# Performance work log

Measured on AMD Instinct MI355X. Metric: run time of the kernel, lower is better.

The kernel has to match this reference:

```python
import jax, jax.numpy as jnp
import numpy as np

B, N, D, KD = 8, 2048, 64, 64

def setup_inputs() -> dict:
    key = jax.random.key(0)
    ks = jax.random.split(key, 7)
    s = 1.0 / np.sqrt(D)
    return {
        "x":  jax.random.normal(ks[0], (B, N, D), dtype=jnp.float32),
        "Wq": jax.random.normal(ks[1], (D, KD), dtype=jnp.float32) * s,
        "bq": jnp.zeros((KD,), jnp.float32),
        "Wk": jax.random.normal(ks[2], (D, KD), dtype=jnp.float32) * s,
        "bk": jnp.zeros((KD,), jnp.float32),
        "Wv": jax.random.normal(ks[3], (D, KD), dtype=jnp.float32) * s,
        "bv": jnp.zeros((KD,), jnp.float32),
    }

def reference(x, Wq, bq, Wk, bk, Wv, bv):
    # Q,K,V: [B,N,KD]
    Q = x @ Wq + bq
    K = x @ Wk + bk
    V = x @ Wv + bv
    # scores: [B,N,N] (note: original applies NO 1/sqrt(d) scaling)
    scores = jnp.einsum('bij,bkj->bik', Q, K)
    probs = jax.nn.softmax(scores, axis=-1)
    # mean-threshold sparsification: keep entries above the row mean
    mask = (probs > jnp.mean(probs, axis=-1, keepdims=True)).astype(probs.dtype)
    sparse = probs * mask
    out = jnp.einsum('bij,bjk->bik', sparse, V)  # [B,N,KD]
    return out
```

## Files before the change

kernel.cpp:

```cpp
#include <hip/hip_runtime.h>

#define NB 8
#define NS 2048
#define ND 64
#define LOG2E 1.44269504f
#define QSC 256.0f
#define IQS (1.0f / 256.0f)

#define KST 80
#define VST 136
#define KTILE (128 * KST)
#define VTILE (64 * VST)

typedef _Float16 half8 __attribute__((ext_vector_type(8)));
typedef _Float16 half4 __attribute__((ext_vector_type(4)));
typedef __attribute__((ext_vector_type(4))) float floatx4;

__device__ __forceinline__ half8 cvt8(const float* p) {
    float4 a = *(const float4*)p;
    float4 b = *(const float4*)(p + 4);
    half8 h = {(_Float16)a.x, (_Float16)a.y, (_Float16)a.z, (_Float16)a.w,
               (_Float16)b.x, (_Float16)b.y, (_Float16)b.z, (_Float16)b.w};
    return h;
}

__global__ __launch_bounds__(256) void wprep(
    const float* __restrict__ Wq, const float* __restrict__ Wk,
    const float* __restrict__ Wv, _Float16* __restrict__ Wt)
{
    const int m = blockIdx.x;
    const float* W = (m == 0) ? Wq : (m == 1) ? Wk : Wv;
    for (int i = threadIdx.x; i < 64 * 64; i += 256) {
        const int c = i >> 6, d = i & 63;
        Wt[((size_t)m * 64 + c) * 64 + d] = (_Float16)W[d * 64 + c];
    }
}

__global__ __launch_bounds__(256) void qkv_proj(
    const float* __restrict__ x, const _Float16* __restrict__ Wt,
    const float* __restrict__ bq, const float* __restrict__ bk,
    const float* __restrict__ bv,
    _Float16* __restrict__ Qg, _Float16* __restrict__ Kg,
    _Float16* __restrict__ Vt)
{
    __shared__ _Float16 vt[4][64 * 20];

    const int tid  = threadIdx.x;
    const int wv   = tid >> 6;
    const int l    = tid & 63;
    const int quad = l >> 4;
    const int tx   = l & 15;

    const int b  = blockIdx.x & 7;
    const int n0 = (blockIdx.x >> 3) * 64 + wv * 16;

    const float* xr = x + ((size_t)b * NS + n0 + tx) * ND + quad * 8;
    half8 a0 = cvt8(xr);
    half8 a1 = cvt8(xr + 32);

    const floatx4 zf = {0.f, 0.f, 0.f, 0.f};

#pragma unroll
    for (int ctile = 0; ctile < 12; ++ctile) {
        const int m    = ctile >> 2;
        const int lcol = (ctile & 3) * 16 + tx;

        const _Float16* Wb = Wt + ((size_t)m * 64 + lcol) * 64;
        half8 b0 = *(const half8*)(Wb + quad * 8);
        half8 b1 = *(const half8*)(Wb + 32 + quad * 8);

        floatx4 acc = __builtin_amdgcn_mfma_f32_16x16x32_f16(a0, b0, zf, 0, 0, 0);
        acc = __builtin_amdgcn_mfma_f32_16x16x32_f16(a1, b1, acc, 0, 0, 0);

        const float* Bp = (m == 0) ? bq : (m == 1) ? bk : bv;
        const float bias = Bp[lcol];

        if (m == 0) {
#pragma unroll
            for (int r = 0; r < 4; ++r)
                Qg[((size_t)b * NS + n0 + quad * 4 + r) * ND + lcol] =
                    (_Float16)((acc[r] + bias) * LOG2E);
        } else if (m == 1) {
#pragma unroll
            for (int r = 0; r < 4; ++r)
                Kg[((size_t)b * NS + n0 + quad * 4 + r) * ND + lcol] =
                    (_Float16)(acc[r] + bias);
        } else {
#pragma unroll
            for (int r = 0; r < 4; ++r)
                vt[wv][lcol * 20 + quad * 4 + r] = (_Float16)(acc[r] + bias);
        }
    }
    __syncthreads();
    {
        const int d = l;
        const _Float16* src = &vt[wv][d * 20];
        uint2 p0 = *(const uint2*)(src);
        uint2 p1 = *(const uint2*)(src + 4);
        uint2 p2 = *(const uint2*)(src + 8);
        uint2 p3 = *(const uint2*)(src + 12);
        uint4 q0 = {p0.x, p0.y, p1.x, p1.y};
        uint4 q1 = {p2.x, p2.y, p3.x, p3.y};
        _Float16* dst = Vt + ((size_t)b * ND + d) * NS + n0;
        *(uint4*)(dst)     = q0;
        *(uint4*)(dst + 8) = q1;
    }
}

__global__ __launch_bounds__(512, 4) void attn(
    const _Float16* __restrict__ Qg,
    const _Float16* __restrict__ Kg,
    const _Float16* __restrict__ Vt,
    float* __restrict__ out)
{
    __shared__ __align__(16) _Float16 smem[2 * KTILE];
    __shared__ float lsh[4 * 32];

    const int tid  = threadIdx.x;
    const int wv   = tid >> 6;
    const int l    = tid & 63;
    const int quad = l >> 4;
    const int tx   = l & 15;
    const int rh   = wv >> 2;
    const int kq   = wv & 3;

    const int b  = blockIdx.x & 7;
    const int q0 = (blockIdx.x >> 3) * 32;

    const _Float16* Qb = Qg + ((size_t)b * NS + q0 + rh * 16) * ND;
    const _Float16* Kb = Kg + (size_t)b * NS * ND;
    const _Float16* Vb = Vt + (size_t)b * ND * NS;

    half8 qf[2];
#pragma unroll
    for (int kc = 0; kc < 2; ++kc)
        qf[kc] = *(const half8*)(Qb + (size_t)tx * ND + kc * 32 + quad * 8);

    const floatx4 zf = {0.f, 0.f, 0.f, 0.f};

    uint2 sr[32];

    float lacc = 0.f;
    {
        const int skey = tid >> 2;
        const int sc0  = tid & 3;
        const _Float16* Ksrc = Kb + (size_t)skey * ND + sc0 * 8;
        const int kd = skey * KST + sc0 * 8;

        uint4 ga = *(const uint4*)Ksrc;
        uint4 gb = *(const uint4*)(Ksrc + 32);
        *(uint4*)(smem + kd) = ga;
        *(uint4*)(smem + kd + 32) = gb;

#pragma unroll
        for (int t = 0; t < 16; ++t) {
            const int buf = (t & 1) * KTILE;
            __syncthreads();
            if (t < 15) {
                ga = *(const uint4*)(Ksrc + (size_t)(t + 1) * 128 * ND);
                gb = *(const uint4*)(Ksrc + (size_t)(t + 1) * 128 * ND + 32);
            }
#pragma unroll
            for (int g = 0; g < 2; ++g) {
                const int krow = buf + (kq * 32 + g * 16 + tx) * KST;
                half8 kf0 = *(const half8*)(smem + krow + quad * 8);
                half8 kf1 = *(const half8*)(smem + krow + 32 + quad * 8);
                floatx4 c = __builtin_amdgcn_mfma_f32_16x16x32_f16(kf0, qf[0], zf, 0, 0, 0);
                c = __builtin_amdgcn_mfma_f32_16x16x32_f16(kf1, qf[1], c, 0, 0, 0);
                int ic[4];
#pragma unroll
                for (int r = 0; r < 4; ++r) {
                    float cs = fminf(fmaxf(c[r] * QSC, -32000.f), 32000.f);
                    int v = (int)rintf(cs);
                    ic[r] = v;
                    lacc += __builtin_amdgcn_exp2f((float)v * IQS);
                }
                sr[t * 2 + g].x = (unsigned)(ic[0] & 0xffff) | ((unsigned)ic[1] << 16);
                sr[t * 2 + g].y = (unsigned)(ic[2] & 0xffff) | ((unsigned)ic[3] << 16);
            }
            if (t < 15) {
                *(uint4*)(smem + (buf ^ KTILE) + kd) = ga;
                *(uint4*)(smem + (buf ^ KTILE) + kd + 32) = gb;
            }
        }
    }
#pragma unroll
    for (int off = 16; off < 64; off <<= 1)
        lacc += __shfl_xor(lacc, off);
    if (quad == 0)
        lsh[kq * 32 + rh * 16 + tx] = lacc;

    const int sdim = tid >> 3;
    const int sv0  = tid & 7;
    const _Float16* Vsrc = Vb + (size_t)sdim * NS + sv0 * 8;
    const int vd = sdim * VST + sv0 * 8;

    uint4 gva = *(const uint4*)Vsrc;
    uint4 gvb = *(const uint4*)(Vsrc + 64);
    __syncthreads();

    float thr, inv;
    {
        const int row = rh * 16 + tx;
        float L = lsh[row] + lsh[32 + row] + lsh[64 + row] + lsh[96 + row];
        inv = 1.f / L;
        thr = L * (1.f / (float)NS);
    }

    *(uint4*)(smem + vd) = gva;
    *(uint4*)(smem + vd + 64) = gvb;

    floatx4 o[4] = {zf, zf, zf, zf};

#pragma unroll
    for (int t = 0; t < 16; ++t) {
        const int buf = (t & 1) * VTILE;
        __syncthreads();
        if (t < 15) {
            gva = *(const uint4*)(Vsrc + (size_t)(t + 1) * 128);
            gvb = *(const uint4*)(Vsrc + (size_t)(t + 1) * 128 + 64);
        }
#pragma unroll
        for (int g = 0; g < 2; ++g) {
            const uint2 u = sr[t * 2 + g];
            int s0 = (int)(short)(u.x), s1 = (int)(short)(u.x >> 16);
            int s2 = (int)(short)(u.y), s3 = (int)(short)(u.y >> 16);
            float e0 = __builtin_amdgcn_exp2f((float)s0 * IQS);
            float e1 = __builtin_amdgcn_exp2f((float)s1 * IQS);
            float e2 = __builtin_amdgcn_exp2f((float)s2 * IQS);
            float e3 = __builtin_amdgcn_exp2f((float)s3 * IQS);
            float w0 = (e0 > thr) ? e0 * inv : 0.f;
            float w1 = (e1 > thr) ? e1 * inv : 0.f;
            float w2 = (e2 > thr) ? e2 * inv : 0.f;
            float w3 = (e3 > thr) ? e3 * inv : 0.f;
            half4 af = {(_Float16)w0, (_Float16)w1, (_Float16)w2, (_Float16)w3};
#pragma unroll
            for (int dg = 0; dg < 4; ++dg) {
                half4 vf = *(const half4*)(smem + buf + (dg * 16 + tx) * VST +
                                           kq * 32 + g * 16 + quad * 4);
                o[dg] = __builtin_amdgcn_mfma_f32_16x16x16f16(af, vf, o[dg], 0, 0, 0);
            }
        }
        if (t < 15) {
            *(uint4*)(smem + (buf ^ VTILE) + vd) = gva;
            *(uint4*)(smem + (buf ^ VTILE) + vd + 64) = gvb;
        }
    }

    __syncthreads();
    float* osm = (float*)smem;
    const int orow = rh * 16 + quad * 4;
    if (kq == 0) {
#pragma unroll
        for (int dg = 0; dg < 4; ++dg)
#pragma unroll
            for (int r = 0; r < 4; ++r)
                osm[(orow + r) * 68 + dg * 16 + tx] = o[dg][r];
    }
    __syncthreads();
    if (kq == 1) {
#pragma unroll
        for (int dg = 0; dg < 4; ++dg)
#pragma unroll
            for (int r = 0; r < 4; ++r)
                osm[(orow + r) * 68 + dg * 16 + tx] += o[dg][r];
    }
    __syncthreads();
    if (kq == 2) {
#pragma unroll
        for (int dg = 0; dg < 4; ++dg)
#pragma unroll
            for (int r = 0; r < 4; ++r)
                osm[(orow + r) * 68 + dg * 16 + tx] += o[dg][r];
    }
    __syncthreads();
    if (kq == 3) {
#pragma unroll
        for (int dg = 0; dg < 4; ++dg)
#pragma unroll
            for (int r = 0; r < 4; ++r)
                out[((size_t)b * NS + q0 + orow + r) * ND + dg * 16 + tx] =
                    osm[(orow + r) * 68 + dg * 16 + tx] + o[dg][r];
    }
}

extern "C" void kernel_launch(void* const* d_in, const int* in_sizes, int n_in,
                              void* d_out, int out_size, void* d_ws, size_t ws_size,
                              hipStream_t stream) {
    const float* x  = (const float*)d_in[0];
    const float* Wq = (const float*)d_in[1];
    const float* bq = (const float*)d_in[2];
    const float* Wk = (const float*)d_in[3];
    const float* bk = (const float*)d_in[4];
    const float* Wv = (const float*)d_in[5];
    const float* bv = (const float*)d_in[6];

    _Float16* Qg = (_Float16*)d_ws;
    _Float16* Kg = Qg + (size_t)NB * NS * ND;
    _Float16* Vt = Kg + (size_t)NB * NS * ND;
    _Float16* Wt = Vt + (size_t)NB * NS * ND;

    wprep<<<3, 256, 0, stream>>>(Wq, Wk, Wv, Wt);
    qkv_proj<<<NB * (NS / 64), 256, 0, stream>>>(x, Wt, bq, bk, bv, Qg, Kg, Vt);
    attn<<<NB * (NS / 32), 512, 0, stream>>>(Qg, Kg, Vt, (float*)d_out);
}
```

Measured before the change: 132.6 us.

## Shrink attention blocks to 16 query rows split across eight key waves

```diff
diff --git a/kernel.cpp b/kernel.cpp
--- a/kernel.cpp
+++ b/kernel.cpp
@@ -15,6 +15,7 @@
 typedef _Float16 half8 __attribute__((ext_vector_type(8)));
 typedef _Float16 half4 __attribute__((ext_vector_type(4)));
 typedef __attribute__((ext_vector_type(4))) float floatx4;
+typedef unsigned uintx16 __attribute__((ext_vector_type(16)));
 
 __device__ __forceinline__ half8 cvt8(const float* p) {
     float4 a = *(const float4*)p;
@@ -114,20 +115,18 @@
     float* __restrict__ out)
 {
     __shared__ __align__(16) _Float16 smem[2 * KTILE];
-    __shared__ float lsh[4 * 32];
+    __shared__ float lsh[8 * 16];
 
     const int tid  = threadIdx.x;
     const int wv   = tid >> 6;
     const int l    = tid & 63;
     const int quad = l >> 4;
     const int tx   = l & 15;
-    const int rh   = wv >> 2;
-    const int kq   = wv & 3;
 
     const int b  = blockIdx.x & 7;
-    const int q0 = (blockIdx.x >> 3) * 32;
-
-    const _Float16* Qb = Qg + ((size_t)b * NS + q0 + rh * 16) * ND;
+    const int q0 = (blockIdx.x >> 3) * 16;
+
+    const _Float16* Qb = Qg + ((size_t)b * NS + q0) * ND;
     const _Float16* Kb = Kg + (size_t)b * NS * ND;
     const _Float16* Vb = Vt + (size_t)b * ND * NS;
 
@@ -138,7 +137,7 @@
 
     const floatx4 zf = {0.f, 0.f, 0.f, 0.f};
 
-    uint2 sr[32];
+    uintx16 sx, sy;
 
     float lacc = 0.f;
     {
@@ -151,6 +150,8 @@
         uint4 gb = *(const uint4*)(Ksrc + 32);
         *(uint4*)(smem + kd) = ga;
         *(uint4*)(smem + kd + 32) = gb;
+
+        const int krow = (wv * 16 + tx) * KST;
 
 #pragma unroll
         for (int t = 0; t < 16; ++t) {
@@ -160,24 +161,20 @@
                 ga = *(const uint4*)(Ksrc + (size_t)(t + 1) * 128 * ND);
                 gb = *(const uint4*)(Ksrc + (size_t)(t + 1) * 128 * ND + 32);
             }
-#pragma unroll
-            for (int g = 0; g < 2; ++g) {
-                const int krow = buf + (kq * 32 + g * 16 + tx) * KST;
-                half8 kf0 = *(const half8*)(smem + krow + quad * 8);
-                half8 kf1 = *(const half8*)(smem + krow + 32 + quad * 8);
-                floatx4 c = __builtin_amdgcn_mfma_f32_16x16x32_f16(kf0, qf[0], zf, 0, 0, 0);
-                c = __builtin_amdgcn_mfma_f32_16x16x32_f16(kf1, qf[1], c, 0, 0, 0);
-                int ic[4];
-#pragma unroll
-                for (int r = 0; r < 4; ++r) {
-                    float cs = fminf(fmaxf(c[r] * QSC, -32000.f), 32000.f);
-                    int v = (int)rintf(cs);
-                    ic[r] = v;
-                    lacc += __builtin_amdgcn_exp2f((float)v * IQS);
-                }
-                sr[t * 2 + g].x = (unsigned)(ic[0] & 0xffff) | ((unsigned)ic[1] << 16);
-                sr[t * 2 + g].y = (unsigned)(ic[2] & 0xffff) | ((unsigned)ic[3] << 16);
+            half8 kf0 = *(const half8*)(smem + buf + krow + quad * 8);
+            half8 kf1 = *(const half8*)(smem + buf + krow + 32 + quad * 8);
+            floatx4 c = __builtin_amdgcn_mfma_f32_16x16x32_f16(kf0, qf[0], zf, 0, 0, 0);
+            c = __builtin_amdgcn_mfma_f32_16x16x32_f16(kf1, qf[1], c, 0, 0, 0);
+            int ic[4];
+#pragma unroll
+            for (int r = 0; r < 4; ++r) {
+                float cs = fminf(fmaxf(c[r] * QSC, -32000.f), 32000.f);
+                int v = (int)rintf(cs);
+                ic[r] = v;
+                lacc += __builtin_amdgcn_exp2f((float)v * IQS);
             }
+            sx[t] = (unsigned)(ic[0] & 0xffff) | ((unsigned)ic[1] << 16);
+            sy[t] = (unsigned)(ic[2] & 0xffff) | ((unsigned)ic[3] << 16);
             if (t < 15) {
                 *(uint4*)(smem + (buf ^ KTILE) + kd) = ga;
                 *(uint4*)(smem + (buf ^ KTILE) + kd + 32) = gb;
@@ -188,7 +185,7 @@
     for (int off = 16; off < 64; off <<= 1)
         lacc += __shfl_xor(lacc, off);
     if (quad == 0)
-        lsh[kq * 32 + rh * 16 + tx] = lacc;
+        lsh[wv * 16 + tx] = lacc;
 
     const int sdim = tid >> 3;
     const int sv0  = tid & 7;
@@ -201,8 +198,8 @@
 
     float thr, inv;
     {
-        const int row = rh * 16 + tx;
-        float L = lsh[row] + lsh[32 + row] + lsh[64 + row] + lsh[96 + row];
+        float L = lsh[tx] + lsh[16 + tx] + lsh[32 + tx] + lsh[48 + tx]
+                + lsh[64 + tx] + lsh[80 + tx] + lsh[96 + tx] + lsh[112 + tx];
         inv = 1.f / L;
         thr = L * (1.f / (float)NS);
     }
@@ -220,11 +217,10 @@
             gva = *(const uint4*)(Vsrc + (size_t)(t + 1) * 128);
             gvb = *(const uint4*)(Vsrc + (size_t)(t + 1) * 128 + 64);
         }
-#pragma unroll
-        for (int g = 0; g < 2; ++g) {
-            const uint2 u = sr[t * 2 + g];
-            int s0 = (int)(short)(u.x), s1 = (int)(short)(u.x >> 16);
-            int s2 = (int)(short)(u.y), s3 = (int)(short)(u.y >> 16);
+        {
+            const unsigned ux = sx[t], uy = sy[t];
+            int s0 = (int)(short)(ux), s1 = (int)(short)(ux >> 16);
+            int s2 = (int)(short)(uy), s3 = (int)(short)(uy >> 16);
             float e0 = __builtin_amdgcn_exp2f((float)s0 * IQS);
             float e1 = __builtin_amdgcn_exp2f((float)s1 * IQS);
             float e2 = __builtin_amdgcn_exp2f((float)s2 * IQS);
@@ -237,7 +233,7 @@
 #pragma unroll
             for (int dg = 0; dg < 4; ++dg) {
                 half4 vf = *(const half4*)(smem + buf + (dg * 16 + tx) * VST +
-                                           kq * 32 + g * 16 + quad * 4);
+                                           wv * 16 + quad * 4);
                 o[dg] = __builtin_amdgcn_mfma_f32_16x16x16f16(af, vf, o[dg], 0, 0, 0);
             }
         }
@@ -249,8 +245,44 @@
 
     __syncthreads();
     float* osm = (float*)smem;
-    const int orow = rh * 16 + quad * 4;
-    if (kq == 0) {
+    const int orow = quad * 4;
+    if (wv >= 4) {
+        float* s = osm + (size_t)(wv - 4) * 16 * 68;
+#pragma unroll
+        for (int dg = 0; dg < 4; ++dg)
+#pragma unroll
+            for (int r = 0; r < 4; ++r)
+                s[(orow + r) * 68 + dg * 16 + tx] = o[dg][r];
+    }
+    __syncthreads();
+    if (wv < 4) {
+        const float* s = osm + (size_t)wv * 16 * 68;
+#pragma unroll
+        for (int dg = 0; dg < 4; ++dg)
+#pragma unroll
+            for (int r = 0; r < 4; ++r)
+                o[dg][r] += s[(orow + r) * 68 + dg * 16 + tx];
+    }
+    __syncthreads();
+    if (wv == 2 || wv == 3) {
+        float* s = osm + (size_t)(wv - 2) * 16 * 68;
+#pragma unroll
+        for (int dg = 0; dg < 4; ++dg)
+#pragma unroll
+            for (int r = 0; r < 4; ++r)
+                s[(orow + r) * 68 + dg * 16 + tx] = o[dg][r];
+    }
+    __syncthreads();
+    if (wv < 2) {
+        const float* s = osm + (size_t)wv * 16 * 68;
+#pragma unroll
+        for (int dg = 0; dg < 4; ++dg)
+#pragma unroll
+            for (int r = 0; r < 4; ++r)
+                o[dg][r] += s[(orow + r) * 68 + dg * 16 + tx];
+    }
+    __syncthreads();
+    if (wv == 1) {
 #pragma unroll
         for (int dg = 0; dg < 4; ++dg)
 #pragma unroll
@@ -258,29 +290,13 @@
                 osm[(orow + r) * 68 + dg * 16 + tx] = o[dg][r];
     }
     __syncthreads();
-    if (kq == 1) {
-#pragma unroll
-        for (int dg = 0; dg < 4; ++dg)
-#pragma unroll
-            for (int r = 0; r < 4; ++r)
-                osm[(orow + r) * 68 + dg * 16 + tx] += o[dg][r];
-    }
-    __syncthreads();
-    if (kq == 2) {
-#pragma unroll
-        for (int dg = 0; dg < 4; ++dg)
-#pragma unroll
-            for (int r = 0; r < 4; ++r)
-                osm[(orow + r) * 68 + dg * 16 + tx] += o[dg][r];
-    }
-    __syncthreads();
-    if (kq == 3) {
+    if (wv == 0) {
 #pragma unroll
         for (int dg = 0; dg < 4; ++dg)
 #pragma unroll
             for (int r = 0; r < 4; ++r)
                 out[((size_t)b * NS + q0 + orow + r) * ND + dg * 16 + tx] =
-                    osm[(orow + r) * 68 + dg * 16 + tx] + o[dg][r];
+                    o[dg][r] + osm[(orow + r) * 68 + dg * 16 + tx];
     }
 }
 
@@ -302,5 +318,5 @@
 
     wprep<<<3, 256, 0, stream>>>(Wq, Wk, Wv, Wt);
     qkv_proj<<<NB * (NS / 64), 256, 0, stream>>>(x, Wt, bq, bk, bv, Qg, Kg, Vt);
-    attn<<<NB * (NS / 32), 512, 0, stream>>>(Qg, Kg, Vt, (float*)d_out);
-}
+    attn<<<NB * (NS / 16), 512, 0, stream>>>(Qg, Kg, Vt, (float*)d_out);
+}
```

Result: faster. 114.8 us (-13.5%).
